# Optimization experiments

Measured on AMD Instinct MI355X. Metric: run time of the kernel, lower is better.

The kernel has to match this reference:

```python
import jax, jax.numpy as jnp
import numpy as np
import math

SIZE = 4096

def fwht(x, scale):
    """Fast Walsh-Hadamard transform over last dim (power of 2), matching the
    torch reference's butterfly ordering: pair adjacent blocks of growing size."""
    orig_shape = x.shape
    n = orig_shape[-1]
    y = x.reshape(-1, n, 1)  # (B, m, c) with m*c == n
    while y.shape[1] > 1:
        B, m, c = y.shape
        y = y.reshape(B, m // 2, 2, c)
        a = y[:, :, 0, :]
        b = y[:, :, 1, :]
        y = jnp.stack([a + b, a - b], axis=2).reshape(B, m // 2, 2 * c)
    return y.reshape(orig_shape) * scale


def setup_inputs() -> dict:
    key = jax.random.key(0)
    kx, ks = jax.random.split(key)
    x = jax.random.normal(kx, (8192, SIZE), dtype=jnp.float32)
    # randomized Hadamard: seed = bernoulli(0.5)*2 - 1  -> random +/-1 vector
    u = jax.random.uniform(ks, (SIZE,), dtype=jnp.float32)
    seed = jnp.where(u < 0.5, -1.0, 1.0).astype(jnp.float32)
    return {"x": x, "seed": seed}


def reference(x, seed):
    scale = 1.0 / math.sqrt(x.shape[-1])
    y = x * seed  # randomized sign flip per feature
    return fwht(y, scale)
```

## Files before the change

### kernel.cpp

```cpp
#include <hip/hip_runtime.h>


#define N 4096

__global__ __launch_bounds__(64) void fwht64_kernel(
    const float* __restrict__ x,
    const float* __restrict__ seed,
    float* __restrict__ out)
{
    extern __shared__ float lds[];
    const int l = threadIdx.x;
    const long long row = blockIdx.x;

    const float* xr = x + row * (long long)N;
    float* outr = out + row * (long long)N;

    float v[64];

    const float4* x4 = reinterpret_cast<const float4*>(xr) + l * 16;
    const float4* s4 = reinterpret_cast<const float4*>(seed) + l * 16;
#pragma unroll
    for (int q = 0; q < 16; ++q) {
        float4 a = x4[q];
        float4 b = s4[q];
        v[4 * q + 0] = a.x * b.x;
        v[4 * q + 1] = a.y * b.y;
        v[4 * q + 2] = a.z * b.z;
        v[4 * q + 3] = a.w * b.w;
    }

#pragma unroll
    for (int s = 1; s < 64; s <<= 1) {
#pragma unroll
        for (int m = 0; m < 64; ++m) {
            if (!(m & s)) {
                float a = v[m], b = v[m | s];
                v[m]     = a + b;
                v[m | s] = a - b;
            }
        }
    }

    float4* lds4 = reinterpret_cast<float4*>(lds);
#pragma unroll
    for (int q = 0; q < 16; ++q) {
        int qq = q ^ (l & 7);
        lds4[l * 16 + qq] = make_float4(v[4 * q + 0], v[4 * q + 1],
                                        v[4 * q + 2], v[4 * q + 3]);
    }
    __syncthreads();
#pragma unroll
    for (int r = 0; r < 64; ++r) {
        v[r] = lds[64 * r + (l ^ (4 * (r & 7)))];
    }

#pragma unroll
    for (int s = 1; s < 64; s <<= 1) {
#pragma unroll
        for (int m = 0; m < 64; ++m) {
            if (!(m & s)) {
                float a = v[m], b = v[m | s];
                v[m]     = a + b;
                v[m | s] = a - b;
            }
        }
    }

#pragma unroll
    for (int r = 0; r < 64; ++r) {
        outr[64 * r + l] = v[r] * 0.015625f;
    }
}

extern "C" void kernel_launch(void* const* d_in, const int* in_sizes, int n_in,
                              void* d_out, int out_size, void* d_ws, size_t ws_size,
                              hipStream_t stream)
{
    const float* x    = (const float*)d_in[0];
    const float* seed = (const float*)d_in[1];
    float* out        = (float*)d_out;

    const int rows = in_sizes[0] / N;
    dim3 grid(rows), block(64);
    size_t shmem = N * sizeof(float);
    fwht64_kernel<<<grid, block, shmem, stream>>>(x, seed, out);
}
```

Before: 53.04 us.

## Process four rows per block with double-buffered register prefetch

Each 64-thread block now handles four rows instead of one, loading the seed once into registers and software-pipelining the work: the next row's global loads are issued into a second 64-float register buffer while the current row is transformed. The goal is to hide global load latency and amortise the seed load and block launch cost. The price is roughly doubled register pressure (two 64-float buffers plus 64 seed values), which may lower occupancy or cause spills, and a quarter as many blocks, giving the scheduler less parallelism. An extra barrier is added before each LDS write to protect the shared buffer that is reused across rows.

```diff
diff --git a/kernel.cpp b/kernel.cpp
--- a/kernel.cpp
+++ b/kernel.cpp
@@ -3,73 +3,87 @@
 
 #define N 4096
 
-__global__ __launch_bounds__(64) void fwht64_kernel(
+__global__ __launch_bounds__(64) void fwht64_pipe_kernel(
     const float* __restrict__ x,
     const float* __restrict__ seed,
     float* __restrict__ out)
 {
-    extern __shared__ float lds[];
+    __shared__ float lds[N];
     const int l = threadIdx.x;
-    const long long row = blockIdx.x;
+    const long long row0 = (long long)blockIdx.x * 4;
 
-    const float* xr = x + row * (long long)N;
-    float* outr = out + row * (long long)N;
-
-    float v[64];
-
-    const float4* x4 = reinterpret_cast<const float4*>(xr) + l * 16;
     const float4* s4 = reinterpret_cast<const float4*>(seed) + l * 16;
+    float sv[64];
 #pragma unroll
     for (int q = 0; q < 16; ++q) {
-        float4 a = x4[q];
-        float4 b = s4[q];
-        v[4 * q + 0] = a.x * b.x;
-        v[4 * q + 1] = a.y * b.y;
-        v[4 * q + 2] = a.z * b.z;
-        v[4 * q + 3] = a.w * b.w;
+        float4 t = s4[q];
+        sv[4*q+0] = t.x; sv[4*q+1] = t.y; sv[4*q+2] = t.z; sv[4*q+3] = t.w;
     }
 
-#pragma unroll
-    for (int s = 1; s < 64; s <<= 1) {
-#pragma unroll
-        for (int m = 0; m < 64; ++m) {
-            if (!(m & s)) {
-                float a = v[m], b = v[m | s];
-                v[m]     = a + b;
-                v[m | s] = a - b;
-            }
-        }
+    const float4* xb = reinterpret_cast<const float4*>(x)
+                       + row0 * (N / 4) + (long long)l * 16;
+    float4* lds4 = reinterpret_cast<float4*>(lds);
+
+    float va[64], vb[64];
+
+#define LOADROW(dst, r)                                                  \
+    {                                                                    \
+        _Pragma("unroll")                                                \
+        for (int q = 0; q < 16; ++q) {                                   \
+            float4 t = xb[(r) * (N / 4) + q];                            \
+            dst[4*q+0] = t.x; dst[4*q+1] = t.y;                          \
+            dst[4*q+2] = t.z; dst[4*q+3] = t.w;                          \
+        }                                                                \
     }
 
-    float4* lds4 = reinterpret_cast<float4*>(lds);
-#pragma unroll
-    for (int q = 0; q < 16; ++q) {
-        int qq = q ^ (l & 7);
-        lds4[l * 16 + qq] = make_float4(v[4 * q + 0], v[4 * q + 1],
-                                        v[4 * q + 2], v[4 * q + 3]);
-    }
-    __syncthreads();
-#pragma unroll
-    for (int r = 0; r < 64; ++r) {
-        v[r] = lds[64 * r + (l ^ (4 * (r & 7)))];
+#define COMPUTEROW(v, r)                                                 \
+    {                                                                    \
+        _Pragma("unroll")                                                \
+        for (int m = 0; m < 64; ++m) v[m] *= sv[m];                      \
+        _Pragma("unroll")                                                \
+        for (int s = 1; s < 64; s <<= 1) {                               \
+            _Pragma("unroll")                                            \
+            for (int m = 0; m < 64; ++m) if (!(m & s)) {                 \
+                float p0 = v[m], p1 = v[m | s];                          \
+                v[m] = p0 + p1; v[m | s] = p0 - p1;                      \
+            }                                                            \
+        }                                                                \
+        __syncthreads(); \
+        _Pragma("unroll")                                                \
+        for (int q = 0; q < 16; ++q) {                                   \
+            int qq = q ^ (l & 7);                                        \
+            lds4[l * 16 + qq] = make_float4(v[4*q+0], v[4*q+1],          \
+                                            v[4*q+2], v[4*q+3]);         \
+        }                                                                \
+        __syncthreads();                                                 \
+        _Pragma("unroll")                                                \
+        for (int rr = 0; rr < 64; ++rr)                                  \
+            v[rr] = lds[64 * rr + (l ^ (4 * (rr & 7)))];                 \
+        _Pragma("unroll")                                                \
+        for (int s = 1; s < 64; s <<= 1) {                               \
+            _Pragma("unroll")                                            \
+            for (int m = 0; m < 64; ++m) if (!(m & s)) {                 \
+                float p0 = v[m], p1 = v[m | s];                          \
+                v[m] = p0 + p1; v[m | s] = p0 - p1;                      \
+            }                                                            \
+        }                                                                \
+        float* o = out + (row0 + (r)) * (long long)N;                    \
+        _Pragma("unroll")                                                \
+        for (int rr = 0; rr < 64; ++rr)                                  \
+            o[64 * rr + l] = v[rr] * 0.015625f;                          \
     }
 
-#pragma unroll
-    for (int s = 1; s < 64; s <<= 1) {
-#pragma unroll
-        for (int m = 0; m < 64; ++m) {
-            if (!(m & s)) {
-                float a = v[m], b = v[m | s];
-                v[m]     = a + b;
-                v[m | s] = a - b;
-            }
-        }
-    }
+    LOADROW(va, 0)
+    LOADROW(vb, 1)
+    COMPUTEROW(va, 0)
+    LOADROW(va, 2)
+    COMPUTEROW(vb, 1)
+    LOADROW(vb, 3)
+    COMPUTEROW(va, 2)
+    COMPUTEROW(vb, 3)
 
-#pragma unroll
-    for (int r = 0; r < 64; ++r) {
-        outr[64 * r + l] = v[r] * 0.015625f;
-    }
+#undef LOADROW
+#undef COMPUTEROW
 }
 
 extern "C" void kernel_launch(void* const* d_in, const int* in_sizes, int n_in,
@@ -81,7 +95,6 @@
     float* out        = (float*)d_out;
 
     const int rows = in_sizes[0] / N;
-    dim3 grid(rows), block(64);
-    size_t shmem = N * sizeof(float);
-    fwht64_kernel<<<grid, block, shmem, stream>>>(x, seed, out);
+    dim3 grid(rows / 4), block(64);
+    fwht64_pipe_kernel<<<grid, block, 0, stream>>>(x, seed, out);
 }
```

Result: faster. 51.52 us (-2.9%).

## Coalesce global loads and stores via permuted data assignment and LDS transpose

Applied to the files above, without the earlier changes.

Each lane now loads float4s strided across the row, so a wavefront reads contiguous 1 KB chunks instead of each lane reading its own 256-byte segment. The Hadamard index mapping is permuted to match, with a new XOR-swizzled LDS layout for the transpose. The output is staged back through LDS so stores become coalesced float4 nontemporal writes. It also adds a launch-bounds occupancy hint and static shared memory, at the cost of an extra LDS round-trip and barrier.

```diff
diff --git a/kernel.cpp b/kernel.cpp
--- a/kernel.cpp
+++ b/kernel.cpp
@@ -3,30 +3,33 @@
 
 #define N 4096
 
-__global__ __launch_bounds__(64) void fwht64_kernel(
+typedef float f32x4 __attribute__((ext_vector_type(4)));
+
+__global__ __launch_bounds__(64, 3) void fwht_coal_kernel(
     const float* __restrict__ x,
     const float* __restrict__ seed,
     float* __restrict__ out)
 {
-    extern __shared__ float lds[];
+    __shared__ float lds[N];
     const int l = threadIdx.x;
     const long long row = blockIdx.x;
 
-    const float* xr = x + row * (long long)N;
-    float* outr = out + row * (long long)N;
+    const f32x4* x4 = reinterpret_cast<const f32x4*>(x + row * (long long)N);
+    const f32x4* s4 = reinterpret_cast<const f32x4*>(seed);
+    f32x4*       o4 = reinterpret_cast<f32x4*>(out + row * (long long)N);
+    f32x4*     lds4 = reinterpret_cast<f32x4*>(lds);
 
     float v[64];
 
-    const float4* x4 = reinterpret_cast<const float4*>(xr) + l * 16;
-    const float4* s4 = reinterpret_cast<const float4*>(seed) + l * 16;
 #pragma unroll
     for (int q = 0; q < 16; ++q) {
-        float4 a = x4[q];
-        float4 b = s4[q];
-        v[4 * q + 0] = a.x * b.x;
-        v[4 * q + 1] = a.y * b.y;
-        v[4 * q + 2] = a.z * b.z;
-        v[4 * q + 3] = a.w * b.w;
+        f32x4 a = x4[64 * q + l];
+        f32x4 b = s4[64 * q + l];
+        f32x4 p = a * b;
+        v[4 * q + 0] = p[0];
+        v[4 * q + 1] = p[1];
+        v[4 * q + 2] = p[2];
+        v[4 * q + 3] = p[3];
     }
 
 #pragma unroll
@@ -34,24 +37,25 @@
 #pragma unroll
         for (int m = 0; m < 64; ++m) {
             if (!(m & s)) {
-                float a = v[m], b = v[m | s];
-                v[m]     = a + b;
-                v[m | s] = a - b;
+                float p0 = v[m], p1 = v[m | s];
+                v[m]     = p0 + p1;
+                v[m | s] = p0 - p1;
             }
         }
     }
 
-    float4* lds4 = reinterpret_cast<float4*>(lds);
 #pragma unroll
     for (int q = 0; q < 16; ++q) {
-        int qq = q ^ (l & 7);
-        lds4[l * 16 + qq] = make_float4(v[4 * q + 0], v[4 * q + 1],
-                                        v[4 * q + 2], v[4 * q + 3]);
+        f32x4 t;
+        t[0] = v[4 * q + 0]; t[1] = v[4 * q + 1];
+        t[2] = v[4 * q + 2]; t[3] = v[4 * q + 3];
+        lds4[(64 * q + l) ^ (q & 7)] = t;
     }
     __syncthreads();
 #pragma unroll
     for (int r = 0; r < 64; ++r) {
-        v[r] = lds[64 * r + (l ^ (4 * (r & 7)))];
+        int a = (l & 3) | (r << 2) | ((l >> 2) << 8);
+        v[r] = lds[a ^ (((l >> 2) & 7) << 2)];
     }
 
 #pragma unroll
@@ -59,16 +63,26 @@
 #pragma unroll
         for (int m = 0; m < 64; ++m) {
             if (!(m & s)) {
-                float a = v[m], b = v[m | s];
-                v[m]     = a + b;
-                v[m | s] = a - b;
+                float p0 = v[m], p1 = v[m | s];
+                v[m]     = p0 + p1;
+                v[m | s] = p0 - p1;
             }
         }
     }
 
+    __syncthreads();
 #pragma unroll
     for (int r = 0; r < 64; ++r) {
-        outr[64 * r + l] = v[r] * 0.015625f;
+        int a = (l & 3) | (r << 2) | ((l >> 2) << 8);
+        lds[a ^ (((l >> 2) & 7) << 2)] = v[r];
+    }
+    __syncthreads();
+
+#pragma unroll
+    for (int q = 0; q < 16; ++q) {
+        f32x4 t = lds4[(64 * q + l) ^ (q & 7)];
+        t *= 0.015625f;
+        __builtin_nontemporal_store(t, &o4[64 * q + l]);
     }
 }
 
@@ -82,6 +96,5 @@
 
     const int rows = in_sizes[0] / N;
     dim3 grid(rows), block(64);
-    size_t shmem = N * sizeof(float);
-    fwht64_kernel<<<grid, block, shmem, stream>>>(x, seed, out);
+    fwht_coal_kernel<<<grid, block, 0, stream>>>(x, seed, out);
 }
```

Measured after the change: 64.89 us. +22.3%, slower.
